# Performance work log

Measured on AMD Instinct MI355X. Metric: run time of the kernel, lower is better.

Reference implementation:

```python
import jax, jax.numpy as jnp
import numpy as np

N, M, D, U = 4096, 65536, 64, 4  # samples, manifold pts, embed dim, manifold coord dim


def setup_inputs() -> dict:
    key = jax.random.key(0)
    k1, k2, k3, k4 = jax.random.split(key, 4)
    return {
        "X": jax.random.normal(k1, (N, D), dtype=jnp.float32),
        "manifold_ptsX": jax.random.normal(k2, (M, D), dtype=jnp.float32),
        # per-manifold-point first derivatives d sigma / d u_i : [M, U, D]
        "d_ui_sigma": jax.random.normal(k3, (M, U, D), dtype=jnp.float32),
        # per-manifold-point second derivatives d^2 sigma / d u_i d u_j : [M, U, U, D]
        "d_ui_uj_sigma": jax.random.normal(k4, (M, U, U, D), dtype=jnp.float32),
    }


def _nearest_idx(X, pts):
    # Brute-force 1-NN in squared euclidean distance (replaces CPU sklearn KDTree query).
    # but we keep it for exactness of the distance values.
    d2 = (jnp.sum(X * X, axis=1, keepdims=True)
          - 2.0 * (X @ pts.T)
          + jnp.sum(pts * pts, axis=1)[None, :])  # [N, M]
    return jnp.argmin(d2, axis=1)  # [N]


def reference(X, manifold_ptsX, d_ui_sigma, d_ui_uj_sigma):
    # Forward: project each input point to its nearest manifold point.
    I_x = _nearest_idx(X, manifold_ptsX)          # [N]
    x = manifold_ptsX[I_x, :]                     # [N, D]
    return x
```

## Files before the change

kernel.cpp:

```cpp
#include <hip/hip_runtime.h>
#include <math.h>
#include <stdint.h>

#define NQ 4096
#define MP 65536
#define DD 64
#define QT 64
#define STRIPES 8
#define PPB (MP / STRIPES)
#define GPS (PPB / 16)
#define PGROUPS (MP / 16)
#define XGROUPS (NQ / 16)

typedef _Float16 f16;
typedef _Float16 f16x8 __attribute__((ext_vector_type(8)));
typedef float f32x4 __attribute__((ext_vector_type(4)));


__global__ __launch_bounds__(256) void prep_k(const float* __restrict__ P,
                                              const float* __restrict__ X,
                                              f16* __restrict__ PF,
                                              f16* __restrict__ XF,
                                              float* __restrict__ pnh) {
    const int w = threadIdx.x >> 6, lane = threadIdx.x & 63;
    const int n16 = lane & 15, quad = lane >> 4;
    const int task = blockIdx.x * 4 + w;
    const float* src; f16* dst; int g; bool dopn;
    if (task < PGROUPS) { src = P; dst = PF; g = task; dopn = true; }
    else                { src = X; dst = XF; g = task - PGROUPS; dopn = false; }

    const float* row = src + ((size_t)g * 16 + n16) * DD;
    float ss = 0.f;
    #pragma unroll
    for (int kh = 0; kh < 2; ++kh) {
        float4 v0 = *reinterpret_cast<const float4*>(row + kh * 32 + quad * 8);
        float4 v1 = *reinterpret_cast<const float4*>(row + kh * 32 + quad * 8 + 4);
        float vv[8] = {v0.x, v0.y, v0.z, v0.w, v1.x, v1.y, v1.z, v1.w};
        f16x8 h, l;
        #pragma unroll
        for (int j = 0; j < 8; ++j) {
            f16 hh = (f16)vv[j];
            h[j] = hh;
            l[j] = (f16)(vv[j] - (float)hh);
            ss = fmaf(vv[j], vv[j], ss);
        }
        *reinterpret_cast<f16x8*>(dst + ((size_t)(g * 2 + 0) * 2 + kh) * 512 + lane * 8) = h;
        *reinterpret_cast<f16x8*>(dst + ((size_t)(g * 2 + 1) * 2 + kh) * 512 + lane * 8) = l;
    }
    if (dopn) {
        ss += __shfl_xor(ss, 16);
        ss += __shfl_xor(ss, 32);
        if (quad == 0) pnh[g * 16 + n16] = 0.5f * ss;
    }
}

__global__ __launch_bounds__(256, 2) void argmin_k(const f16* __restrict__ PF,
                                                   const f16* __restrict__ XF,
                                                   const float* __restrict__ pnh,
                                                   unsigned long long* __restrict__ best) {
    const int t = threadIdx.x;
    const int lane = t & 63, w = t >> 6;
    const int n16 = lane & 15, quad = lane >> 4;
    const int b = blockIdx.x;
    const int stripe = b & 7;
    const int qBase = (b >> 3) * QT;

    f16x8 QH[4][2], QL[4][2];
    {
        const int qg0 = qBase >> 4;
        #pragma unroll
        for (int nt = 0; nt < 4; ++nt)
            #pragma unroll
            for (int kh = 0; kh < 2; ++kh) {
                const f16* o = XF + ((size_t)(qg0 + nt) * 4 + kh) * 512 + lane * 8;
                QH[nt][kh] = *reinterpret_cast<const f16x8*>(o);
                QL[nt][kh] = *reinterpret_cast<const f16x8*>(o + 1024);
            }
    }

    float rmax[4];
    int   ridx[4];
    #pragma unroll
    for (int nt = 0; nt < 4; ++nt) { rmax[nt] = -INFINITY; ridx[nt] = 0; }

    auto PROC = [&](int gg, f16x8* PH, f16x8* PL) {
        f32x4 pq = *reinterpret_cast<const f32x4*>(pnh + gg * 16 + quad * 4);
        #pragma unroll
        for (int nt = 0; nt < 4; ++nt) {
            f32x4 a = {0.f, 0.f, 0.f, 0.f};
            #pragma unroll
            for (int kh = 0; kh < 2; ++kh) {
                a = __builtin_amdgcn_mfma_f32_16x16x32_f16(PH[kh], QH[nt][kh], a, 0, 0, 0);
                a = __builtin_amdgcn_mfma_f32_16x16x32_f16(PH[kh], QL[nt][kh], a, 0, 0, 0);
                a = __builtin_amdgcn_mfma_f32_16x16x32_f16(PL[kh], QH[nt][kh], a, 0, 0, 0);
            }
            float s0 = a[0] - pq[0], s1 = a[1] - pq[1];
            float s2 = a[2] - pq[2], s3 = a[3] - pq[3];
            float smax = fmaxf(fmaxf(s0, s1), fmaxf(s2, s3));
            if (smax > rmax[nt]) {
                rmax[nt] = smax;
                int r = 3;
                r = (s2 == smax) ? 2 : r;
                r = (s1 == smax) ? 1 : r;
                r = (s0 == smax) ? 0 : r;
                ridx[nt] = gg * 16 + quad * 4 + r;
            }
        }
    };

    int g = stripe * GPS + w;
    f16x8 PHa[2], PLa[2], PHb[2], PLb[2];
    {
        const f16* f0 = PF + (size_t)g * 2048 + lane * 8;
        PHa[0] = *reinterpret_cast<const f16x8*>(f0);
        PHa[1] = *reinterpret_cast<const f16x8*>(f0 + 512);
        PLa[0] = *reinterpret_cast<const f16x8*>(f0 + 1024);
        PLa[1] = *reinterpret_cast<const f16x8*>(f0 + 1536);
    }
    for (int i = 0; i < GPS / 4; i += 2) {
        {
            const f16* fn = PF + (size_t)(g + 4) * 2048 + lane * 8;
            PHb[0] = *reinterpret_cast<const f16x8*>(fn);
            PHb[1] = *reinterpret_cast<const f16x8*>(fn + 512);
            PLb[0] = *reinterpret_cast<const f16x8*>(fn + 1024);
            PLb[1] = *reinterpret_cast<const f16x8*>(fn + 1536);
        }
        PROC(g, PHa, PLa);
        {
            int gp = (i + 2 < GPS / 4) ? g + 8 : g;
            const f16* fn = PF + (size_t)gp * 2048 + lane * 8;
            PHa[0] = *reinterpret_cast<const f16x8*>(fn);
            PHa[1] = *reinterpret_cast<const f16x8*>(fn + 512);
            PLa[0] = *reinterpret_cast<const f16x8*>(fn + 1024);
            PLa[1] = *reinterpret_cast<const f16x8*>(fn + 1536);
        }
        PROC(g + 4, PHb, PLb);
        g += 8;
    }

    #pragma unroll
    for (int nt = 0; nt < 4; ++nt) {
        float sv = rmax[nt]; int iv = ridx[nt];
        #pragma unroll
        for (int m = 16; m < 64; m <<= 1) {
            float so = __shfl_xor(sv, m);
            int   io = __shfl_xor(iv, m);
            if (so > sv || (so == sv && io < iv)) { sv = so; iv = io; }
        }
        if (quad == 0) {
            float s = -2.f * sv;
            unsigned u = __float_as_uint(s);
            u = (u & 0x80000000u) ? ~u : (u | 0x80000000u);
            unsigned long long key = ((unsigned long long)u << 32) | (unsigned)iv;
            atomicMin(&best[qBase + nt * 16 + n16], key);
        }
    }
}

__global__ __launch_bounds__(256) void gather_k(const unsigned long long* __restrict__ best,
                                                const float* __restrict__ P,
                                                float* __restrict__ out) {
    int g = blockIdx.x * 256 + threadIdx.x;
    int q = g >> 4, c = g & 15;
    unsigned idx = (unsigned)best[q];
    reinterpret_cast<float4*>(out)[g] =
        reinterpret_cast<const float4*>(P)[(size_t)idx * 16 + c];
}

extern "C" void kernel_launch(void* const* d_in, const int* in_sizes, int n_in,
                              void* d_out, int out_size, void* d_ws, size_t ws_size,
                              hipStream_t stream) {
    const float* X = (const float*)d_in[0];
    const float* P = (const float*)d_in[1];
    float* out = (float*)d_out;

    unsigned long long* best = (unsigned long long*)d_ws;
    float* pnh = (float*)((char*)d_ws + 32768);
    f16*   XF  = (f16*)((char*)d_ws + 294912);
    f16*   PF  = (f16*)((char*)d_ws + 1343488);

    hipMemsetAsync(d_ws, 0xFF, NQ * sizeof(unsigned long long), stream);

    prep_k<<<(PGROUPS + XGROUPS) / 4, 256, 0, stream>>>(P, X, PF, XF, pnh);

    argmin_k<<<(NQ / QT) * STRIPES, 256, 0, stream>>>(PF, XF, pnh, best);

    gather_k<<<NQ * 16 / 256, 256, 0, stream>>>(best, P, out);
}
```

Before: 419.7 us.

## Switch argmin to 32x32x16 MFMA tiles with bias-initialized accumulators

Moves the split-fp16 distance GEMM from 16x16x32 to 32x32x16 MFMA, changing the packed data layout in prep to 32-row groups. The negated half-norm is loaded straight into the accumulator so no separate subtraction is needed, and s_setprio is placed around the MFMA chain. Initialising the best array moves from a memset into the prep kernel, which removes one launch. In exchange each lane holds 16 accumulator values and scans them for the argmax, which raises register pressure and may affect occupancy.

```diff
diff --git a/kernel.cpp b/kernel.cpp
--- a/kernel.cpp
+++ b/kernel.cpp
@@ -8,33 +8,35 @@
 #define QT 64
 #define STRIPES 8
 #define PPB (MP / STRIPES)
-#define GPS (PPB / 16)
-#define PGROUPS (MP / 16)
-#define XGROUPS (NQ / 16)
+#define GPS32 (PPB / 32)
+#define PG32 (MP / 32)
+#define XG32 (NQ / 32)
 
 typedef _Float16 f16;
 typedef _Float16 f16x8 __attribute__((ext_vector_type(8)));
 typedef float f32x4 __attribute__((ext_vector_type(4)));
+typedef float f32x16 __attribute__((ext_vector_type(16)));
 
 
 __global__ __launch_bounds__(256) void prep_k(const float* __restrict__ P,
                                               const float* __restrict__ X,
                                               f16* __restrict__ PF,
                                               f16* __restrict__ XF,
-                                              float* __restrict__ pnh) {
+                                              float* __restrict__ pnh,
+                                              unsigned long long* __restrict__ best) {
     const int w = threadIdx.x >> 6, lane = threadIdx.x & 63;
-    const int n16 = lane & 15, quad = lane >> 4;
+    const int r32 = lane & 31, hi = lane >> 5;
     const int task = blockIdx.x * 4 + w;
-    const float* src; f16* dst; int g; bool dopn;
-    if (task < PGROUPS) { src = P; dst = PF; g = task; dopn = true; }
-    else                { src = X; dst = XF; g = task - PGROUPS; dopn = false; }
+    const float* src; f16* dst; int g; bool isP;
+    if (task < PG32) { src = P; dst = PF; g = task; isP = true; }
+    else             { src = X; dst = XF; g = task - PG32; isP = false; }
 
-    const float* row = src + ((size_t)g * 16 + n16) * DD;
+    const float* row = src + ((size_t)g * 32 + r32) * DD;
     float ss = 0.f;
     #pragma unroll
-    for (int kh = 0; kh < 2; ++kh) {
-        float4 v0 = *reinterpret_cast<const float4*>(row + kh * 32 + quad * 8);
-        float4 v1 = *reinterpret_cast<const float4*>(row + kh * 32 + quad * 8 + 4);
+    for (int t = 0; t < 4; ++t) {
+        float4 v0 = *reinterpret_cast<const float4*>(row + t * 16 + hi * 8);
+        float4 v1 = *reinterpret_cast<const float4*>(row + t * 16 + hi * 8 + 4);
         float vv[8] = {v0.x, v0.y, v0.z, v0.w, v1.x, v1.y, v1.z, v1.w};
         f16x8 h, l;
         #pragma unroll
@@ -44,13 +46,15 @@
             l[j] = (f16)(vv[j] - (float)hh);
             ss = fmaf(vv[j], vv[j], ss);
         }
-        *reinterpret_cast<f16x8*>(dst + ((size_t)(g * 2 + 0) * 2 + kh) * 512 + lane * 8) = h;
-        *reinterpret_cast<f16x8*>(dst + ((size_t)(g * 2 + 1) * 2 + kh) * 512 + lane * 8) = l;
+        *reinterpret_cast<f16x8*>(dst + (((size_t)g * 2 + 0) * 4 + t) * 512 + lane * 8) = h;
+        *reinterpret_cast<f16x8*>(dst + (((size_t)g * 2 + 1) * 4 + t) * 512 + lane * 8) = l;
     }
-    if (dopn) {
-        ss += __shfl_xor(ss, 16);
+    if (isP) {
         ss += __shfl_xor(ss, 32);
-        if (quad == 0) pnh[g * 16 + n16] = 0.5f * ss;
+        if (hi == 0) pnh[g * 32 + r32] = -0.5f * ss;
+    } else {
+        int q = g * 64 + lane;
+        if (q < NQ) best[q] = 0xFFFFFFFFFFFFFFFFULL;
     }
 }
 
@@ -60,99 +64,100 @@
                                                    unsigned long long* __restrict__ best) {
     const int t = threadIdx.x;
     const int lane = t & 63, w = t >> 6;
-    const int n16 = lane & 15, quad = lane >> 4;
+    const int col = lane & 31, hi = lane >> 5;
     const int b = blockIdx.x;
     const int stripe = b & 7;
     const int qBase = (b >> 3) * QT;
 
-    f16x8 QH[4][2], QL[4][2];
+    f16x8 QH[2][4], QL[2][4];
     {
-        const int qg0 = qBase >> 4;
+        const int qg0 = qBase >> 5;
         #pragma unroll
-        for (int nt = 0; nt < 4; ++nt)
+        for (int nt = 0; nt < 2; ++nt)
             #pragma unroll
-            for (int kh = 0; kh < 2; ++kh) {
-                const f16* o = XF + ((size_t)(qg0 + nt) * 4 + kh) * 512 + lane * 8;
-                QH[nt][kh] = *reinterpret_cast<const f16x8*>(o);
-                QL[nt][kh] = *reinterpret_cast<const f16x8*>(o + 1024);
+            for (int k = 0; k < 4; ++k) {
+                const f16* o = XF + (size_t)(qg0 + nt) * 4096 + k * 512 + lane * 8;
+                QH[nt][k] = *reinterpret_cast<const f16x8*>(o);
+                QL[nt][k] = *reinterpret_cast<const f16x8*>(o + 2048);
             }
     }
 
-    float rmax[4];
-    int   ridx[4];
-    #pragma unroll
-    for (int nt = 0; nt < 4; ++nt) { rmax[nt] = -INFINITY; ridx[nt] = 0; }
+    float rmax[2] = {-INFINITY, -INFINITY};
+    int   ridx[2] = {0, 0};
 
-    auto PROC = [&](int gg, f16x8* PH, f16x8* PL) {
-        f32x4 pq = *reinterpret_cast<const f32x4*>(pnh + gg * 16 + quad * 4);
+    auto LOADG = [&](int gg, f16x8* PH, f16x8* PL, f32x4* B) {
+        const f16* f0 = PF + (size_t)gg * 4096 + lane * 8;
         #pragma unroll
-        for (int nt = 0; nt < 4; ++nt) {
-            f32x4 a = {0.f, 0.f, 0.f, 0.f};
+        for (int k = 0; k < 4; ++k) {
+            PH[k] = *reinterpret_cast<const f16x8*>(f0 + k * 512);
+            PL[k] = *reinterpret_cast<const f16x8*>(f0 + 2048 + k * 512);
+        }
+        const float* pb = pnh + gg * 32 + hi * 4;
+        #pragma unroll
+        for (int rr = 0; rr < 4; ++rr)
+            B[rr] = *reinterpret_cast<const f32x4*>(pb + rr * 8);
+    };
+
+    auto PROC = [&](int gg, f16x8* PH, f16x8* PL, f32x4* B) {
+        #pragma unroll
+        for (int nt = 0; nt < 2; ++nt) {
+            f32x16 a;
             #pragma unroll
-            for (int kh = 0; kh < 2; ++kh) {
-                a = __builtin_amdgcn_mfma_f32_16x16x32_f16(PH[kh], QH[nt][kh], a, 0, 0, 0);
-                a = __builtin_amdgcn_mfma_f32_16x16x32_f16(PH[kh], QL[nt][kh], a, 0, 0, 0);
-                a = __builtin_amdgcn_mfma_f32_16x16x32_f16(PL[kh], QH[nt][kh], a, 0, 0, 0);
+            for (int rr = 0; rr < 4; ++rr) {
+                a[rr * 4 + 0] = B[rr][0]; a[rr * 4 + 1] = B[rr][1];
+                a[rr * 4 + 2] = B[rr][2]; a[rr * 4 + 3] = B[rr][3];
             }
-            float s0 = a[0] - pq[0], s1 = a[1] - pq[1];
-            float s2 = a[2] - pq[2], s3 = a[3] - pq[3];
-            float smax = fmaxf(fmaxf(s0, s1), fmaxf(s2, s3));
+            __builtin_amdgcn_s_setprio(1);
+            #pragma unroll
+            for (int k = 0; k < 4; ++k) {
+                a = __builtin_amdgcn_mfma_f32_32x32x16_f16(PH[k], QH[nt][k], a, 0, 0, 0);
+                a = __builtin_amdgcn_mfma_f32_32x32x16_f16(PH[k], QL[nt][k], a, 0, 0, 0);
+                a = __builtin_amdgcn_mfma_f32_32x32x16_f16(PL[k], QH[nt][k], a, 0, 0, 0);
+            }
+            __builtin_amdgcn_s_setprio(0);
+            float m0 = fmaxf(fmaxf(a[0], a[1]),  fmaxf(a[2], a[3]));
+            float m1 = fmaxf(fmaxf(a[4], a[5]),  fmaxf(a[6], a[7]));
+            float m2 = fmaxf(fmaxf(a[8], a[9]),  fmaxf(a[10], a[11]));
+            float m3 = fmaxf(fmaxf(a[12], a[13]), fmaxf(a[14], a[15]));
+            float smax = fmaxf(fmaxf(m0, m1), fmaxf(m2, m3));
+            int rsel = 15;
+            #pragma unroll
+            for (int r = 14; r >= 0; --r) rsel = (a[r] == smax) ? r : rsel;
             if (smax > rmax[nt]) {
                 rmax[nt] = smax;
-                int r = 3;
-                r = (s2 == smax) ? 2 : r;
-                r = (s1 == smax) ? 1 : r;
-                r = (s0 == smax) ? 0 : r;
-                ridx[nt] = gg * 16 + quad * 4 + r;
+                ridx[nt] = gg * 32 + (rsel & 3) + 8 * (rsel >> 2) + 4 * hi;
             }
         }
     };
 
-    int g = stripe * GPS + w;
-    f16x8 PHa[2], PLa[2], PHb[2], PLb[2];
-    {
-        const f16* f0 = PF + (size_t)g * 2048 + lane * 8;
-        PHa[0] = *reinterpret_cast<const f16x8*>(f0);
-        PHa[1] = *reinterpret_cast<const f16x8*>(f0 + 512);
-        PLa[0] = *reinterpret_cast<const f16x8*>(f0 + 1024);
-        PLa[1] = *reinterpret_cast<const f16x8*>(f0 + 1536);
-    }
-    for (int i = 0; i < GPS / 4; i += 2) {
+    int g = stripe * GPS32 + w;
+    f16x8 PHa[4], PLa[4], PHb[4], PLb[4];
+    f32x4 Ba[4], Bb[4];
+    LOADG(g, PHa, PLa, Ba);
+    #pragma unroll 1
+    for (int i = 0; i < GPS32 / 4; i += 2) {
+        LOADG(g + 4, PHb, PLb, Bb);
+        PROC(g, PHa, PLa, Ba);
         {
-            const f16* fn = PF + (size_t)(g + 4) * 2048 + lane * 8;
-            PHb[0] = *reinterpret_cast<const f16x8*>(fn);
-            PHb[1] = *reinterpret_cast<const f16x8*>(fn + 512);
-            PLb[0] = *reinterpret_cast<const f16x8*>(fn + 1024);
-            PLb[1] = *reinterpret_cast<const f16x8*>(fn + 1536);
+            int gp = (i + 2 < GPS32 / 4) ? g + 8 : g;
+            LOADG(gp, PHa, PLa, Ba);
         }
-        PROC(g, PHa, PLa);
-        {
-            int gp = (i + 2 < GPS / 4) ? g + 8 : g;
-            const f16* fn = PF + (size_t)gp * 2048 + lane * 8;
-            PHa[0] = *reinterpret_cast<const f16x8*>(fn);
-            PHa[1] = *reinterpret_cast<const f16x8*>(fn + 512);
-            PLa[0] = *reinterpret_cast<const f16x8*>(fn + 1024);
-            PLa[1] = *reinterpret_cast<const f16x8*>(fn + 1536);
-        }
-        PROC(g + 4, PHb, PLb);
+        PROC(g + 4, PHb, PLb, Bb);
         g += 8;
     }
 
     #pragma unroll
-    for (int nt = 0; nt < 4; ++nt) {
+    for (int nt = 0; nt < 2; ++nt) {
         float sv = rmax[nt]; int iv = ridx[nt];
-        #pragma unroll
-        for (int m = 16; m < 64; m <<= 1) {
-            float so = __shfl_xor(sv, m);
-            int   io = __shfl_xor(iv, m);
-            if (so > sv || (so == sv && io < iv)) { sv = so; iv = io; }
-        }
-        if (quad == 0) {
+        float so = __shfl_xor(sv, 32);
+        int   io = __shfl_xor(iv, 32);
+        if (so > sv || (so == sv && io < iv)) { sv = so; iv = io; }
+        if (hi == 0) {
             float s = -2.f * sv;
             unsigned u = __float_as_uint(s);
             u = (u & 0x80000000u) ? ~u : (u | 0x80000000u);
             unsigned long long key = ((unsigned long long)u << 32) | (unsigned)iv;
-            atomicMin(&best[qBase + nt * 16 + n16], key);
+            atomicMin(&best[qBase + nt * 32 + col], key);
         }
     }
 }
@@ -179,9 +184,7 @@
     f16*   XF  = (f16*)((char*)d_ws + 294912);
     f16*   PF  = (f16*)((char*)d_ws + 1343488);
 
-    hipMemsetAsync(d_ws, 0xFF, NQ * sizeof(unsigned long long), stream);
-
-    prep_k<<<(PGROUPS + XGROUPS) / 4, 256, 0, stream>>>(P, X, PF, XF, pnh);
+    prep_k<<<(PG32 + XG32) / 4, 256, 0, stream>>>(P, X, PF, XF, pnh, best);
 
     argmin_k<<<(NQ / QT) * STRIPES, 256, 0, stream>>>(PF, XF, pnh, best);
 
```

Result: no change. 426.1 us (+1.5%).
